# Performance work log

Measured on AMD Instinct MI355X. Metric: run time of the kernel, lower is better.

## Reference

```python
import jax, jax.numpy as jnp
import numpy as np

# dims
B, S, D, DS = 4, 4096, 2048, 64
NF, NR, NT = 4096, 2048, 2048  # feature / relational / transfer neuron pools
KF, KR, KT = 8, 4, 6           # top-k per pool


def setup_inputs() -> dict:
    key = jax.random.key(0)
    k1, k2, k3, k4 = jax.random.split(key, 4)
    x = jax.random.normal(k1, (B, S, D), dtype=jnp.float32)
    importance = jax.random.uniform(k2, (B, S), dtype=jnp.float32)
    proj_w = jax.random.normal(k3, (D, DS), dtype=jnp.float32) * 0.02
    proj_b = jnp.zeros((DS,), dtype=jnp.float32)
    neuron_emb = jax.random.normal(k4, (NF + NR + NT, DS), dtype=jnp.float32) * 0.02
    return {"x": x, "importance": importance, "proj_w": proj_w,
            "proj_b": proj_b, "neuron_emb": neuron_emb}


def _topk_sparsify(w, k):
    # top-k along last dim, scatter back, renormalize (matches _topk_sparsify)
    vals, idx = jax.lax.top_k(w, k)                      # [B,k]
    rows = jnp.arange(w.shape[0])[:, None]
    sparse = jnp.zeros_like(w).at[rows, idx].set(vals)   # [B,N]
    return sparse / (sparse.sum(axis=-1, keepdims=True) + 1e-8)


def reference(x, importance, proj_w, proj_b, neuron_emb):
    # eval mode: dropout off, no excitability bias, no aux loss
    h = x @ proj_w + proj_b                               # [B,S,DS]
    norm = jnp.maximum(jnp.linalg.norm(neuron_emb, axis=-1, keepdims=True), 1e-12)
    emb = neuron_emb / norm                               # F.normalize
    logits = jnp.einsum('bsd,nd->bsn', h, emb)            # [B,S,NF+NR+NT]

    feat_pref = jax.nn.softmax(logits[..., :NF], axis=-1)
    relQ_pref = jax.nn.softmax(logits[..., NF:NF + NR], axis=-1)
    relK_pref = jax.nn.softmax(logits[..., NF:NF + NR], axis=-1)
    tran_pref = jax.nn.softmax(logits[..., NF + NR:], axis=-1)

    # importance-weighted pooling over tokens -> dense per-batch routing weights
    fw = _topk_sparsify(jnp.einsum('bs,bsn->bn', importance, feat_pref), KF)
    qw = _topk_sparsify(jnp.einsum('bs,bsn->bn', importance, relQ_pref), KR)
    kw = _topk_sparsify(jnp.einsum('bs,bsn->bn', importance, relK_pref), KR)
    tw = _topk_sparsify(jnp.einsum('bs,bsn->bn', importance, tran_pref), KT)

    return jnp.concatenate([fw, qw, kw, tw], axis=-1)     # [B, NF+2*NR+NT]
```

## Files before the change

kernel.cpp:

```cpp
#include <hip/hip_runtime.h>
#include <math.h>

#define BATCH 4
#define SEQ   4096
#define DIM   2048
#define DS    64
#define NF    4096
#define NR    2048
#define NT    2048
#define NTOT  8192
#define TOK   16384
#define KSPLIT 4

typedef __attribute__((ext_vector_type(8))) __bf16 bf16x8;
typedef __attribute__((ext_vector_type(4))) float  f32x4;

static __device__ __forceinline__ unsigned short f2bf(float x) {
  unsigned int u = __float_as_uint(x);
  u += 0x7fffu + ((u >> 16) & 1u);
  return (unsigned short)(u >> 16);
}
static __device__ __forceinline__ float bf2f(unsigned int lo16) {
  return __uint_as_float(lo16 << 16);
}

__global__ __launch_bounds__(256) void k_prep_emb(const float* __restrict__ emb,
                                                  unsigned short* __restrict__ eh,
                                                  unsigned short* __restrict__ el) {
  int row  = blockIdx.x * 4 + (threadIdx.x >> 6);
  int lane = threadIdx.x & 63;
  float v  = emb[(size_t)row * DS + lane];
  float ss = v * v;
#pragma unroll
  for (int m = 32; m >= 1; m >>= 1) ss += __shfl_xor(ss, m, 64);
  float sc = 1.0f / fmaxf(sqrtf(ss), 1e-12f);
  float w  = v * sc;
  unsigned short hi = f2bf(w);
  eh[(size_t)row * DS + lane] = hi;
  el[(size_t)row * DS + lane] = f2bf(w - bf2f(hi));
}

__global__ __launch_bounds__(256) void k_prep_w(const float* __restrict__ W,
                                                unsigned short* __restrict__ wth,
                                                unsigned short* __restrict__ wtl) {
  int c = blockIdx.x;
#pragma unroll
  for (int it = 0; it < 8; ++it) {
    int k = threadIdx.x + it * 256;
    float v = W[(size_t)k * DS + c];
    unsigned short hi = f2bf(v);
    wth[(size_t)c * DIM + k] = hi;
    wtl[(size_t)c * DIM + k] = f2bf(v - bf2f(hi));
  }
}

__global__ __launch_bounds__(256) void k_h(
    const float* __restrict__ x, const unsigned short* __restrict__ wth,
    const unsigned short* __restrict__ wtl, float* __restrict__ Hpart) {
  __shared__ __align__(16) unsigned short xh[2][64 * 32];
  __shared__ __align__(16) unsigned short xl[2][64 * 32];
  __shared__ __align__(16) unsigned short wh[2][64 * 32];
  __shared__ __align__(16) unsigned short wl[2][64 * 32];
  const int tid  = threadIdx.x;
  const int t0   = blockIdx.x * 64;
  const int kbase = blockIdx.y * (DIM / KSPLIT);
  const int lane = tid & 63, wv = tid >> 6;
  const int fr   = lane & 15, oct = lane >> 4;

  float4 xrA[2], xrB[2];
  uint4  wrA[2], wrB[2];

  auto LOADX = [&](int k0, float4* xr, uint4* wr) {
#pragma unroll
    for (int it = 0; it < 2; ++it) {
      int idx = tid + it * 256;
      int r = idx >> 3, q = idx & 7;
      xr[it] = *reinterpret_cast<const float4*>(
          &x[(size_t)(t0 + r) * DIM + k0 + q * 4]);
    }
    int c = tid >> 2, s = tid & 3;
    size_t bo = ((size_t)c * DIM + k0 + s * 8) * 2;
    wr[0] = *reinterpret_cast<const uint4*>((const char*)wth + bo);
    wr[1] = *reinterpret_cast<const uint4*>((const char*)wtl + bo);
  };
  auto STORE = [&](int buf, float4* xr, uint4* wr) {
#pragma unroll
    for (int it = 0; it < 2; ++it) {
      int idx = tid + it * 256;
      int r = idx >> 3, q = idx & 7;
      int bo = (r * 64 + q * 8) ^ ((r & 3) << 4);
      float4 v = xr[it];
      unsigned short a0 = f2bf(v.x), a1 = f2bf(v.y), a2 = f2bf(v.z), a3 = f2bf(v.w);
      uint2 hi; hi.x = a0 | ((unsigned)a1 << 16); hi.y = a2 | ((unsigned)a3 << 16);
      *reinterpret_cast<uint2*>((char*)xh[buf] + bo) = hi;
      uint2 lo;
      lo.x = (unsigned)f2bf(v.x - bf2f(a0)) | ((unsigned)f2bf(v.y - bf2f(a1)) << 16);
      lo.y = (unsigned)f2bf(v.z - bf2f(a2)) | ((unsigned)f2bf(v.w - bf2f(a3)) << 16);
      *reinterpret_cast<uint2*>((char*)xl[buf] + bo) = lo;
    }
    int c = tid >> 2, s = tid & 3;
    int bo = (c * 64 + s * 16) ^ ((c & 3) << 4);
    *reinterpret_cast<uint4*>((char*)wh[buf] + bo) = wr[0];
    *reinterpret_cast<uint4*>((char*)wl[buf] + bo) = wr[1];
  };

  f32x4 acc[4];
#pragma unroll
  for (int j = 0; j < 4; ++j) acc[j] = (f32x4)0.0f;

  auto COMPUTE = [&](int buf) {
    int row = wv * 16 + fr;
    int boA = (row * 64 + oct * 16) ^ ((row & 3) << 4);
    bf16x8 ah  = *reinterpret_cast<const bf16x8*>((const char*)xh[buf] + boA);
    bf16x8 al_ = *reinterpret_cast<const bf16x8*>((const char*)xl[buf] + boA);
#pragma unroll
    for (int j = 0; j < 4; ++j) {
      int c = j * 16 + fr;
      int boB = (c * 64 + oct * 16) ^ ((c & 3) << 4);
      bf16x8 bh  = *reinterpret_cast<const bf16x8*>((const char*)wh[buf] + boB);
      bf16x8 bl_ = *reinterpret_cast<const bf16x8*>((const char*)wl[buf] + boB);
      acc[j] = __builtin_amdgcn_mfma_f32_16x16x32_bf16(ah,  bh,  acc[j], 0, 0, 0);
      acc[j] = __builtin_amdgcn_mfma_f32_16x16x32_bf16(ah,  bl_, acc[j], 0, 0, 0);
      acc[j] = __builtin_amdgcn_mfma_f32_16x16x32_bf16(al_, bh,  acc[j], 0, 0, 0);
    }
  };

  LOADX(kbase, xrA, wrA);
  LOADX(kbase + 32, xrB, wrB);
  for (int s = 0; s < 16; s += 2) {
    STORE(0, xrA, wrA);
    if (s + 2 < 16) LOADX(kbase + (s + 2) * 32, xrA, wrA);
    __syncthreads();
    COMPUTE(0);
    STORE(1, xrB, wrB);
    if (s + 3 < 16) LOADX(kbase + (s + 3) * 32, xrB, wrB);
    __syncthreads();
    COMPUTE(1);
  }

  float* op = Hpart + (size_t)blockIdx.y * TOK * DS;
#pragma unroll
  for (int j = 0; j < 4; ++j) {
    int c = j * 16 + fr;
#pragma unroll
    for (int r = 0; r < 4; ++r) {
      int t = t0 + wv * 16 + oct * 4 + r;
      op[(size_t)t * DS + c] = acc[j][r];
    }
  }
}

__global__ __launch_bounds__(256) void k_hc(const float* __restrict__ Hpart,
                                            const float* __restrict__ bias,
                                            unsigned short* __restrict__ hh,
                                            unsigned short* __restrict__ hl) {
  int idx = blockIdx.x * 256 + threadIdx.x;
  int t = idx >> 4, q = idx & 15;
  size_t o = (size_t)t * DS + q * 4;
  float4 s0 = *reinterpret_cast<const float4*>(&Hpart[o]);
  float4 s1 = *reinterpret_cast<const float4*>(&Hpart[(size_t)TOK * DS + o]);
  float4 s2 = *reinterpret_cast<const float4*>(&Hpart[2 * (size_t)TOK * DS + o]);
  float4 s3 = *reinterpret_cast<const float4*>(&Hpart[3 * (size_t)TOK * DS + o]);
  float4 bv = *reinterpret_cast<const float4*>(&bias[q * 4]);
  float v0 = (s0.x + s1.x) + (s2.x + s3.x) + bv.x;
  float v1 = (s0.y + s1.y) + (s2.y + s3.y) + bv.y;
  float v2 = (s0.z + s1.z) + (s2.z + s3.z) + bv.z;
  float v3 = (s0.w + s1.w) + (s2.w + s3.w) + bv.w;
  unsigned short h0 = f2bf(v0), h1 = f2bf(v1), h2 = f2bf(v2), h3 = f2bf(v3);
  uint2 hi; hi.x = h0 | ((unsigned)h1 << 16); hi.y = h2 | ((unsigned)h3 << 16);
  uint2 lo;
  lo.x = (unsigned)f2bf(v0 - bf2f(h0)) | ((unsigned)f2bf(v1 - bf2f(h1)) << 16);
  lo.y = (unsigned)f2bf(v2 - bf2f(h2)) | ((unsigned)f2bf(v3 - bf2f(h3)) << 16);
  *reinterpret_cast<uint2*>(&hh[o]) = hi;
  *reinterpret_cast<uint2*>(&hl[o]) = lo;
}

template<int MODE>
__global__ __launch_bounds__(256, 3) void k_zle(
    const unsigned short* __restrict__ hh, const unsigned short* __restrict__ hl,
    const unsigned short* __restrict__ eh, const unsigned short* __restrict__ el,
    const float* __restrict__ a, float* __restrict__ Zp, float* __restrict__ Bp) {
  __shared__ __align__(16) unsigned short esh[128 * 64];
  __shared__ __align__(16) unsigned short esl[128 * 64];
  __shared__ float red2[512];
  const int tid = threadIdx.x;
  const int tb  = blockIdx.x;
  const int cb  = blockIdx.y;
  const int t0  = tb * 128;

  const int lane = tid & 63;
  const int wv   = tid >> 6;
  const int fr   = lane & 15;
  const int oct  = lane >> 4;

  bf16x8 ah[2][2], al[2][2];
#pragma unroll
  for (int i = 0; i < 2; ++i)
#pragma unroll
    for (int kh = 0; kh < 2; ++kh) {
      size_t off = (size_t)(t0 + wv * 32 + i * 16 + fr) * DS + kh * 32 + oct * 8;
      ah[i][kh] = *reinterpret_cast<const bf16x8*>(hh + off);
      al[i][kh] = *reinterpret_cast<const bf16x8*>(hl + off);
    }

  float av[2][4];
  if (MODE == 2) {
    const int sl = (cb < 8) ? 0 : ((cb < 12) ? 1 : 2);
#pragma unroll
    for (int i = 0; i < 2; ++i)
#pragma unroll
      for (int r = 0; r < 4; ++r)
        av[i][r] = a[(size_t)sl * TOK + t0 + wv * 32 + i * 16 + oct * 4 + r];
  }
  float rs[2][4];
#pragma unroll
  for (int i = 0; i < 2; ++i)
#pragma unroll
    for (int r = 0; r < 4; ++r) rs[i][r] = 0.0f;

  for (int sub = 0; sub < 4; ++sub) {
    const int n0 = cb * 512 + sub * 128;
    if (sub) __syncthreads();
#pragma unroll
    for (int it = 0; it < 4; ++it) {
      int idx = tid + it * 256;
      int r = idx >> 3, k8 = idx & 7;
      int bo = (r * 128 + k8 * 16) ^ ((r & 7) << 4);
      *reinterpret_cast<uint4*>((char*)esh + bo) =
          *reinterpret_cast<const uint4*>((const char*)eh + (size_t)(n0 + r) * 128 + k8 * 16);
      *reinterpret_cast<uint4*>((char*)esl + bo) =
          *reinterpret_cast<const uint4*>((const char*)el + (size_t)(n0 + r) * 128 + k8 * 16);
    }
    __syncthreads();

    f32x4 acc[2][8];
#pragma unroll
    for (int i = 0; i < 2; ++i)
#pragma unroll
      for (int j = 0; j < 8; ++j) acc[i][j] = (f32x4)0.0f;

#pragma unroll
    for (int j = 0; j < 8; ++j) {
      int col = j * 16 + fr;
      bf16x8 bh[2], bl[2];
#pragma unroll
      for (int kh = 0; kh < 2; ++kh) {
        int bo = (col * 128 + (kh * 32 + oct * 8) * 2) ^ ((col & 7) << 4);
        bh[kh] = *reinterpret_cast<const bf16x8*>((const char*)esh + bo);
        bl[kh] = *reinterpret_cast<const bf16x8*>((const char*)esl + bo);
      }
#pragma unroll
      for (int i = 0; i < 2; ++i) {
#pragma unroll
        for (int kh = 0; kh < 2; ++kh) {
          acc[i][j] = __builtin_amdgcn_mfma_f32_16x16x32_bf16(ah[i][kh], bh[kh], acc[i][j], 0, 0, 0);
          acc[i][j] = __builtin_amdgcn_mfma_f32_16x16x32_bf16(ah[i][kh], bl[kh], acc[i][j], 0, 0, 0);
          acc[i][j] = __builtin_amdgcn_mfma_f32_16x16x32_bf16(al[i][kh], bh[kh], acc[i][j], 0, 0, 0);
        }
      }
    }

    if (MODE == 0) {
#pragma unroll
      for (int i = 0; i < 2; ++i)
#pragma unroll
        for (int j = 0; j < 8; ++j)
#pragma unroll
          for (int r = 0; r < 4; ++r) rs[i][r] += __expf(acc[i][j][r]);
    } else {
      float cs[8];
#pragma unroll
      for (int j = 0; j < 8; ++j) {
        float s = 0.0f;
#pragma unroll
        for (int i = 0; i < 2; ++i)
#pragma unroll
          for (int r = 0; r < 4; ++r) s = fmaf(av[i][r], __expf(acc[i][j][r]), s);
        cs[j] = s;
      }
#pragma unroll
      for (int j = 0; j < 8; ++j) {
        cs[j] += __shfl_xor(cs[j], 16, 64);
        cs[j] += __shfl_xor(cs[j], 32, 64);
      }
      if (oct == 0) {
#pragma unroll
        for (int j = 0; j < 8; ++j) red2[wv * 128 + j * 16 + fr] = cs[j];
      }
      __syncthreads();
      if (tid < 128) {
        float v = red2[tid] + red2[128 + tid] + red2[256 + tid] + red2[384 + tid];
        Bp[(size_t)tb * NTOT + n0 + tid] = v;
      }
    }
  }

  if (MODE == 0) {
#pragma unroll
    for (int m = 1; m < 16; m <<= 1)
#pragma unroll
      for (int i = 0; i < 2; ++i)
#pragma unroll
        for (int r = 0; r < 4; ++r) rs[i][r] += __shfl_xor(rs[i][r], m, 64);
    if (fr == 0) {
#pragma unroll
      for (int i = 0; i < 2; ++i)
#pragma unroll
        for (int r = 0; r < 4; ++r) {
          int t = t0 + wv * 32 + i * 16 + oct * 4 + r;
          Zp[(size_t)t * 16 + cb] = rs[i][r];
        }
    }
  }
}

__global__ __launch_bounds__(256) void k_a2(const float* __restrict__ Zp,
                                            const float* __restrict__ imp,
                                            float* __restrict__ a) {
  int t = blockIdx.x * 256 + threadIdx.x;
  const float4* zp = reinterpret_cast<const float4*>(&Zp[(size_t)t * 16]);
  float4 q0 = zp[0], q1 = zp[1], q2 = zp[2], q3 = zp[3];
  float zf = ((q0.x + q0.y) + (q0.z + q0.w)) + ((q1.x + q1.y) + (q1.z + q1.w));
  float zr = (q2.x + q2.y) + (q2.z + q2.w);
  float zt = (q3.x + q3.y) + (q3.z + q3.w);
  float im = imp[t];
  a[t]           = im / zf;
  a[TOK + t]     = im / zr;
  a[2 * TOK + t] = im / zt;
}

__global__ __launch_bounds__(256) void k_red(const float* __restrict__ Bp,
                                             float* __restrict__ pooled) {
  int idx = blockIdx.x * 256 + threadIdx.x;
  int b = idx >> 13;
  int n = idx & (NTOT - 1);
  const float* src = Bp + (size_t)(b * 32) * NTOT + n;
  float s = 0.0f;
#pragma unroll
  for (int g = 0; g < 32; ++g) s += src[(size_t)g * NTOT];
  pooled[idx] = s;
}

__global__ __launch_bounds__(256) void k_topk(const float* __restrict__ pooled,
                                              float* __restrict__ out) {
  __shared__ float p[4096];
  __shared__ float rv[256];
  __shared__ int   ri[256];
  __shared__ float vals[8];
  __shared__ int   idxs[8];
  __shared__ float s_inv;

  const int bid = blockIdx.x;
  const int b   = bid / 3;
  const int sl  = bid % 3;
  const int off = (sl == 0) ? 0 : ((sl == 1) ? NF : NF + NR);
  const int N   = (sl == 0) ? NF : NR;
  const int K   = (sl == 0) ? 8 : ((sl == 1) ? 4 : 6);
  const int tid = threadIdx.x;

  for (int i = tid; i < N; i += 256)
    p[i] = pooled[(size_t)b * NTOT + off + i];
  __syncthreads();

  for (int k = 0; k < K; ++k) {
    float bv = -2.0f;
    int bi = 1 << 30;
    for (int i = tid; i < N; i += 256) {
      float v = p[i];
      if (v > bv) { bv = v; bi = i; }
    }
    rv[tid] = bv; ri[tid] = bi;
    __syncthreads();
    for (int st = 128; st > 0; st >>= 1) {
      if (tid < st) {
        float v2 = rv[tid + st]; int i2 = ri[tid + st];
        if (v2 > rv[tid] || (v2 == rv[tid] && i2 < ri[tid])) {
          rv[tid] = v2; ri[tid] = i2;
        }
      }
      __syncthreads();
    }
    if (tid == 0) {
      vals[k] = rv[0]; idxs[k] = ri[0];
      p[ri[0]] = -1.0f;
    }
    __syncthreads();
  }

  if (tid == 0) {
    float s = 0.0f;
    for (int k = 0; k < K; ++k) s += vals[k];
    s_inv = 1.0f / (s + 1e-8f);
  }
  __syncthreads();

  float* ob = out + (size_t)b * (NF + 2 * NR + NT);
  if (sl == 0) {
    for (int i = tid; i < NF; i += 256) ob[i] = 0.0f;
  } else if (sl == 1) {
    for (int i = tid; i < NR; i += 256) { ob[NF + i] = 0.0f; ob[NF + NR + i] = 0.0f; }
  } else {
    for (int i = tid; i < NT; i += 256) ob[NF + 2 * NR + i] = 0.0f;
  }
  __syncthreads();
  if (tid < K) {
    float v = vals[tid] * s_inv;
    int ix = idxs[tid];
    if (sl == 0) {
      ob[ix] = v;
    } else if (sl == 1) {
      ob[NF + ix] = v;
      ob[NF + NR + ix] = v;
    } else {
      ob[NF + 2 * NR + ix] = v;
    }
  }
}

extern "C" void kernel_launch(void* const* d_in, const int* in_sizes, int n_in,
                              void* d_out, int out_size, void* d_ws, size_t ws_size,
                              hipStream_t stream) {
  const float* x    = (const float*)d_in[0];
  const float* imp  = (const float*)d_in[1];
  const float* W    = (const float*)d_in[2];
  const float* bias = (const float*)d_in[3];
  const float* emb  = (const float*)d_in[4];
  float* out = (float*)d_out;

  unsigned short* eh  = (unsigned short*)d_ws;
  unsigned short* el  = eh  + (size_t)NTOT * DS;
  unsigned short* wth = el  + (size_t)NTOT * DS;
  unsigned short* wtl = wth + (size_t)DS * DIM;
  unsigned short* hh  = wtl + (size_t)DS * DIM;
  unsigned short* hl  = hh  + (size_t)TOK * DS;
  float* Zp     = (float*)(hl + (size_t)TOK * DS);
  float* a      = Zp + (size_t)TOK * 16;
  float* Bp     = a + 3 * (size_t)TOK;
  float* pooled = Bp + (size_t)128 * NTOT;
  float* Hpart  = pooled + (size_t)BATCH * NTOT;

  size_t need = (2 * (size_t)NTOT * DS + 2 * (size_t)DS * DIM +
                 2 * (size_t)TOK * DS) * sizeof(unsigned short) +
                ((size_t)TOK * 16 + 3 * (size_t)TOK + 128 * (size_t)NTOT +
                 (size_t)BATCH * NTOT + (size_t)KSPLIT * TOK * DS) * sizeof(float);
  if (ws_size < need) return;

  k_prep_emb<<<NTOT / 4, 256, 0, stream>>>(emb, eh, el);
  k_prep_w<<<DS, 256, 0, stream>>>(W, wth, wtl);
  k_h<<<dim3(TOK / 64, KSPLIT), 256, 0, stream>>>(x, wth, wtl, Hpart);
  k_hc<<<TOK * 16 / 256, 256, 0, stream>>>(Hpart, bias, hh, hl);

  k_zle<0><<<dim3(128, 16), 256, 0, stream>>>(hh, hl, eh, el, nullptr, Zp, nullptr);
  k_a2<<<TOK / 256, 256, 0, stream>>>(Zp, imp, a);
  k_zle<2><<<dim3(128, 16), 256, 0, stream>>>(hh, hl, eh, el, a, nullptr, Bp);
  k_red<<<(BATCH * NTOT) / 256, 256, 0, stream>>>(Bp, pooled);
  k_topk<<<12, 256, 0, stream>>>(pooled, out);
}
```

Before: 190.4 us.

## Stage full W slice in LDS and stream x directly into MFMA registers

```diff
diff --git a/kernel.cpp b/kernel.cpp
--- a/kernel.cpp
+++ b/kernel.cpp
@@ -10,7 +10,8 @@
 #define NT    2048
 #define NTOT  8192
 #define TOK   16384
-#define KSPLIT 4
+#define KSPLIT 8
+#define KS    (DIM / KSPLIT)
 
 typedef __attribute__((ext_vector_type(8))) __bf16 bf16x8;
 typedef __attribute__((ext_vector_type(4))) float  f32x4;
@@ -22,6 +23,19 @@
 }
 static __device__ __forceinline__ float bf2f(unsigned int lo16) {
   return __uint_as_float(lo16 << 16);
+}
+
+static __device__ __forceinline__ void split8(const float4& a, const float4& b,
+                                              bf16x8& hi, bf16x8& lo) {
+  float v[8] = {a.x, a.y, a.z, a.w, b.x, b.y, b.z, b.w};
+  union { unsigned short u[8]; bf16x8 v8; } H, L;
+#pragma unroll
+  for (int i = 0; i < 8; ++i) {
+    unsigned short h = f2bf(v[i]);
+    H.u[i] = h;
+    L.u[i] = f2bf(v[i] - bf2f(h));
+  }
+  hi = H.v8; lo = L.v8;
 }
 
 __global__ __launch_bounds__(256) void k_prep_emb(const float* __restrict__ emb,
@@ -54,88 +68,57 @@
   }
 }
 
-__global__ __launch_bounds__(256) void k_h(
+__global__ __launch_bounds__(512) void k_h(
     const float* __restrict__ x, const unsigned short* __restrict__ wth,
     const unsigned short* __restrict__ wtl, float* __restrict__ Hpart) {
-  __shared__ __align__(16) unsigned short xh[2][64 * 32];
-  __shared__ __align__(16) unsigned short xl[2][64 * 32];
-  __shared__ __align__(16) unsigned short wh[2][64 * 32];
-  __shared__ __align__(16) unsigned short wl[2][64 * 32];
-  const int tid  = threadIdx.x;
-  const int t0   = blockIdx.x * 64;
-  const int kbase = blockIdx.y * (DIM / KSPLIT);
-  const int lane = tid & 63, wv = tid >> 6;
-  const int fr   = lane & 15, oct = lane >> 4;
-
-  float4 xrA[2], xrB[2];
-  uint4  wrA[2], wrB[2];
-
-  auto LOADX = [&](int k0, float4* xr, uint4* wr) {
-#pragma unroll
-    for (int it = 0; it < 2; ++it) {
-      int idx = tid + it * 256;
-      int r = idx >> 3, q = idx & 7;
-      xr[it] = *reinterpret_cast<const float4*>(
-          &x[(size_t)(t0 + r) * DIM + k0 + q * 4]);
-    }
-    int c = tid >> 2, s = tid & 3;
-    size_t bo = ((size_t)c * DIM + k0 + s * 8) * 2;
-    wr[0] = *reinterpret_cast<const uint4*>((const char*)wth + bo);
-    wr[1] = *reinterpret_cast<const uint4*>((const char*)wtl + bo);
-  };
-  auto STORE = [&](int buf, float4* xr, uint4* wr) {
-#pragma unroll
-    for (int it = 0; it < 2; ++it) {
-      int idx = tid + it * 256;
-      int r = idx >> 3, q = idx & 7;
-      int bo = (r * 64 + q * 8) ^ ((r & 3) << 4);
-      float4 v = xr[it];
-      unsigned short a0 = f2bf(v.x), a1 = f2bf(v.y), a2 = f2bf(v.z), a3 = f2bf(v.w);
-      uint2 hi; hi.x = a0 | ((unsigned)a1 << 16); hi.y = a2 | ((unsigned)a3 << 16);
-      *reinterpret_cast<uint2*>((char*)xh[buf] + bo) = hi;
-      uint2 lo;
-      lo.x = (unsigned)f2bf(v.x - bf2f(a0)) | ((unsigned)f2bf(v.y - bf2f(a1)) << 16);
-      lo.y = (unsigned)f2bf(v.z - bf2f(a2)) | ((unsigned)f2bf(v.w - bf2f(a3)) << 16);
-      *reinterpret_cast<uint2*>((char*)xl[buf] + bo) = lo;
-    }
-    int c = tid >> 2, s = tid & 3;
-    int bo = (c * 64 + s * 16) ^ ((c & 3) << 4);
-    *reinterpret_cast<uint4*>((char*)wh[buf] + bo) = wr[0];
-    *reinterpret_cast<uint4*>((char*)wl[buf] + bo) = wr[1];
-  };
+  __shared__ __align__(16) unsigned short wsh[64 * KS];
+  __shared__ __align__(16) unsigned short wsl[64 * KS];
+  const int tid   = threadIdx.x;
+  const int t0    = blockIdx.x * 128;
+  const int kbase = blockIdx.y * KS;
+  const int lane  = tid & 63, wv = tid >> 6;
+  const int fr    = lane & 15, oct = lane >> 4;
+
+#pragma unroll
+  for (int it = 0; it < 4; ++it) {
+    int idx = tid + it * 512;
+    int c = idx >> 5, k16 = idx & 31;
+    int bo = (c * 512 + k16 * 16) ^ ((c & 7) << 4);
+    size_t src = ((size_t)c * DIM + kbase) * 2 + (size_t)k16 * 16;
+    *reinterpret_cast<uint4*>((char*)wsh + bo) =
+        *reinterpret_cast<const uint4*>((const char*)wth + src);
+    *reinterpret_cast<uint4*>((char*)wsl + bo) =
+        *reinterpret_cast<const uint4*>((const char*)wtl + src);
+  }
+  __syncthreads();
+
+  const float* xp = x + (size_t)(t0 + wv * 16 + fr) * DIM + kbase + oct * 8;
 
   f32x4 acc[4];
 #pragma unroll
   for (int j = 0; j < 4; ++j) acc[j] = (f32x4)0.0f;
 
-  auto COMPUTE = [&](int buf) {
-    int row = wv * 16 + fr;
-    int boA = (row * 64 + oct * 16) ^ ((row & 3) << 4);
-    bf16x8 ah  = *reinterpret_cast<const bf16x8*>((const char*)xh[buf] + boA);
-    bf16x8 al_ = *reinterpret_cast<const bf16x8*>((const char*)xl[buf] + boA);
+  float4 xa = *reinterpret_cast<const float4*>(xp);
+  float4 xb = *reinterpret_cast<const float4*>(xp + 4);
+
+#pragma unroll
+  for (int s = 0; s < KS / 32; ++s) {
+    bf16x8 ah, al;
+    split8(xa, xb, ah, al);
+    if (s + 1 < KS / 32) {
+      xa = *reinterpret_cast<const float4*>(xp + (s + 1) * 32);
+      xb = *reinterpret_cast<const float4*>(xp + (s + 1) * 32 + 4);
+    }
 #pragma unroll
     for (int j = 0; j < 4; ++j) {
-      int c = j * 16 + fr;
-      int boB = (c * 64 + oct * 16) ^ ((c & 3) << 4);
-      bf16x8 bh  = *reinterpret_cast<const bf16x8*>((const char*)wh[buf] + boB);
-      bf16x8 bl_ = *reinterpret_cast<const bf16x8*>((const char*)wl[buf] + boB);
-      acc[j] = __builtin_amdgcn_mfma_f32_16x16x32_bf16(ah,  bh,  acc[j], 0, 0, 0);
-      acc[j] = __builtin_amdgcn_mfma_f32_16x16x32_bf16(ah,  bl_, acc[j], 0, 0, 0);
-      acc[j] = __builtin_amdgcn_mfma_f32_16x16x32_bf16(al_, bh,  acc[j], 0, 0, 0);
-    }
-  };
-
-  LOADX(kbase, xrA, wrA);
-  LOADX(kbase + 32, xrB, wrB);
-  for (int s = 0; s < 16; s += 2) {
-    STORE(0, xrA, wrA);
-    if (s + 2 < 16) LOADX(kbase + (s + 2) * 32, xrA, wrA);
-    __syncthreads();
-    COMPUTE(0);
-    STORE(1, xrB, wrB);
-    if (s + 3 < 16) LOADX(kbase + (s + 3) * 32, xrB, wrB);
-    __syncthreads();
-    COMPUTE(1);
+      int col = j * 16 + fr;
+      int bo = (col * 512 + s * 64 + oct * 16) ^ ((col & 7) << 4);
+      bf16x8 bh = *reinterpret_cast<const bf16x8*>((const char*)wsh + bo);
+      bf16x8 bl = *reinterpret_cast<const bf16x8*>((const char*)wsl + bo);
+      acc[j] = __builtin_amdgcn_mfma_f32_16x16x32_bf16(ah, bh, acc[j], 0, 0, 0);
+      acc[j] = __builtin_amdgcn_mfma_f32_16x16x32_bf16(ah, bl, acc[j], 0, 0, 0);
+      acc[j] = __builtin_amdgcn_mfma_f32_16x16x32_bf16(al, bh, acc[j], 0, 0, 0);
+    }
   }
 
   float* op = Hpart + (size_t)blockIdx.y * TOK * DS;
@@ -157,15 +140,13 @@
   int idx = blockIdx.x * 256 + threadIdx.x;
   int t = idx >> 4, q = idx & 15;
   size_t o = (size_t)t * DS + q * 4;
-  float4 s0 = *reinterpret_cast<const float4*>(&Hpart[o]);
-  float4 s1 = *reinterpret_cast<const float4*>(&Hpart[(size_t)TOK * DS + o]);
-  float4 s2 = *reinterpret_cast<const float4*>(&Hpart[2 * (size_t)TOK * DS + o]);
-  float4 s3 = *reinterpret_cast<const float4*>(&Hpart[3 * (size_t)TOK * DS + o]);
   float4 bv = *reinterpret_cast<const float4*>(&bias[q * 4]);
-  float v0 = (s0.x + s1.x) + (s2.x + s3.x) + bv.x;
-  float v1 = (s0.y + s1.y) + (s2.y + s3.y) + bv.y;
-  float v2 = (s0.z + s1.z) + (s2.z + s3.z) + bv.z;
-  float v3 = (s0.w + s1.w) + (s2.w + s3.w) + bv.w;
+  float v0 = bv.x, v1 = bv.y, v2 = bv.z, v3 = bv.w;
+#pragma unroll
+  for (int p = 0; p < KSPLIT; ++p) {
+    float4 s = *reinterpret_cast<const float4*>(&Hpart[(size_t)p * TOK * DS + o]);
+    v0 += s.x; v1 += s.y; v2 += s.z; v3 += s.w;
+  }
   unsigned short h0 = f2bf(v0), h1 = f2bf(v1), h2 = f2bf(v2), h3 = f2bf(v3);
   uint2 hi; hi.x = h0 | ((unsigned)h1 << 16); hi.y = h2 | ((unsigned)h3 << 16);
   uint2 lo;
@@ -447,7 +428,7 @@
 
   k_prep_emb<<<NTOT / 4, 256, 0, stream>>>(emb, eh, el);
   k_prep_w<<<DS, 256, 0, stream>>>(W, wth, wtl);
-  k_h<<<dim3(TOK / 64, KSPLIT), 256, 0, stream>>>(x, wth, wtl, Hpart);
+  k_h<<<dim3(TOK / 128, KSPLIT), 512, 0, stream>>>(x, wth, wtl, Hpart);
   k_hc<<<TOK * 16 / 256, 256, 0, stream>>>(Hpart, bias, hh, hl);
 
   k_zle<0><<<dim3(128, 16), 256, 0, stream>>>(hh, hl, eh, el, nullptr, Zp, nullptr);
```

After: 170.0 us. 10.7% less time.
